# Optimization experiments

Measured on AMD Instinct MI355X. Metric: run time of the kernel, lower is better.

Reference implementation:

```python
import jax, jax.numpy as jnp
import numpy as np

DIST_THRES = 0.2
EPS = 1e-8


def _project(points, extrinsic, intrinsic):
    # points: [N,3] world; extrinsic: cam-to-world [4,4]; intrinsic: normalized [3,3]
    w2c = jnp.linalg.inv(extrinsic)
    hom = jnp.concatenate([points, jnp.ones_like(points[:, :1])], axis=-1)  # [N,4]
    cam = hom @ w2c.T  # [N,4]
    z = cam[:, 2]
    valid_z = z > EPS
    xy = cam[:, :2] / jnp.maximum(z, EPS)[:, None]
    ndc = xy @ intrinsic[:2, :2].T + intrinsic[:2, 2]  # [N,2] in [0,1] if visible
    return ndc, valid_z


def _remove_redundancy_batch(means_v, covs_v, shs_v, opas_v, scales_v, rots_v, extr, intr, h, w):
    # means_v: [v,hw,3]; extr: [v,4,4]; intr: [v,3,3]
    v, hw = means_v.shape[0], means_v.shape[1]
    n_total = v * hw
    attrs = (means_v, covs_v, shs_v, opas_v, scales_v, rots_v)

    def init_buf(x):
        buf = jnp.zeros((n_total,) + x.shape[2:], x.dtype)
        return buf.at[:hw].set(x[0])  # view 0 kept wholesale

    bufs = [init_buf(a) for a in attrs]
    valid = jnp.zeros((n_total,), bool).at[:hw].set(True)

    for view in range(1, v):  # small fixed view count: python loop ok
        ndc, vz = _project(bufs[0], extr[view], intr[view])
        m = (ndc[:, 0] >= 0) & (ndc[:, 0] < 1) & (ndc[:, 1] >= 0) & (ndc[:, 1] < 1) & vz & valid
        x = jnp.floor(ndc[:, 0] * w).astype(jnp.int32)
        y = jnp.floor(ndc[:, 1] * h).astype(jnp.int32)
        # original indexes with stride h (y*h + x); bug-faithful, requires h == w
        pix = jnp.clip(y * h + x, 0, hw - 1)
        vpts = means_v[view][pix]  # gather candidate view gaussian at projected pixel
        dist = jnp.linalg.norm(bufs[0] - vpts, axis=1)
        occ = m & (dist <= DIST_THRES)  # accumulated gaussians that cover a pixel of this view
        idx = jnp.where(occ, pix, hw)  # dump masked-out entries into overflow slot
        keep = jnp.ones((hw + 1,), bool).at[idx].set(False)[:hw]  # unoccupied pixels -> keep new gaussian
        sl = slice(view * hw, (view + 1) * hw)
        new_vals = tuple(a[view] for a in attrs)
        bufs = [b.at[sl].set(jnp.where(keep.reshape((-1,) + (1,) * (nv.ndim - 1)), nv, 0))
                for b, nv in zip(bufs, new_vals)]
        valid = valid.at[sl].set(keep)
    return bufs + [valid]


def reference(means, covariances, harmonics, opacities, scales, rotations, extrinsics, intrinsics, h, w):
    b = means.shape[0]
    outs = [
        _remove_redundancy_batch(means[i], covariances[i], harmonics[i], opacities[i],
                                 scales[i], rotations[i], extrinsics[i], intrinsics[i], h, w)
        for i in range(b)
    ]
    # (means, covariances, harmonics, opacities, scales, rotations, valid_mask)
    return tuple(jnp.stack([o[k] for o in outs]) for k in range(7))


def setup_inputs() -> dict:
    key = jax.random.key(0)
    b, v, h, w, d_sh = 1, 4, 256, 256, 25
    hw = h * w
    ks = jax.random.split(key, 7)
    xy = jax.random.uniform(ks[0], (b, v, hw, 2), minval=-1.5, maxval=1.5)
    z = jax.random.uniform(ks[1], (b, v, hw, 1), minval=1.0, maxval=3.0)
    means = jnp.concatenate([xy, z], axis=-1)
    covariances = jax.random.normal(ks[2], (b, v, hw, 3, 3)) * 0.01
    harmonics = jax.random.normal(ks[3], (b, v, hw, 3, d_sh))
    opacities = jax.random.uniform(ks[4], (b, v, hw))
    scales = jax.random.uniform(ks[5], (b, v, hw, 3)) * 0.05
    rotations = jax.random.normal(ks[6], (b, v, hw, 4))
    # near-identity cam-to-world with small x offsets per view
    offs = jnp.arange(v, dtype=jnp.float32) * 0.15 - 0.225
    extrinsics = jnp.tile(jnp.eye(4, dtype=jnp.float32), (b, v, 1, 1)).at[:, :, 0, 3].set(offs[None, :])
    intrinsics = (jnp.zeros((b, v, 3, 3), jnp.float32)
                  .at[:, :, 0, 0].set(1.0).at[:, :, 1, 1].set(1.0)
                  .at[:, :, 0, 2].set(0.5).at[:, :, 1, 2].set(0.5)
                  .at[:, :, 2, 2].set(1.0))
    return {"means": means, "covariances": covariances, "harmonics": harmonics,
            "opacities": opacities, "scales": scales, "rotations": rotations,
            "extrinsics": extrinsics, "intrinsics": intrinsics, "h": h, "w": w}
```

## Files before the change

### kernel.cpp

```cpp
#include <hip/hip_runtime.h>
#include <stdint.h>


__device__ void inv4x4(const float* M, float* out) {
    double m[16];
    for (int i = 0; i < 16; ++i) m[i] = (double)M[i];
    double inv[16];
    inv[0]  =  m[5]*m[10]*m[15] - m[5]*m[11]*m[14] - m[9]*m[6]*m[15] + m[9]*m[7]*m[14] + m[13]*m[6]*m[11] - m[13]*m[7]*m[10];
    inv[4]  = -m[4]*m[10]*m[15] + m[4]*m[11]*m[14] + m[8]*m[6]*m[15] - m[8]*m[7]*m[14] - m[12]*m[6]*m[11] + m[12]*m[7]*m[10];
    inv[8]  =  m[4]*m[9]*m[15]  - m[4]*m[11]*m[13] - m[8]*m[5]*m[15] + m[8]*m[7]*m[13] + m[12]*m[5]*m[11] - m[12]*m[7]*m[9];
    inv[12] = -m[4]*m[9]*m[14]  + m[4]*m[10]*m[13] + m[8]*m[5]*m[14] - m[8]*m[6]*m[13] - m[12]*m[5]*m[10] + m[12]*m[6]*m[9];
    inv[1]  = -m[1]*m[10]*m[15] + m[1]*m[11]*m[14] + m[9]*m[2]*m[15] - m[9]*m[3]*m[14] - m[13]*m[2]*m[11] + m[13]*m[3]*m[10];
    inv[5]  =  m[0]*m[10]*m[15] - m[0]*m[11]*m[14] - m[8]*m[2]*m[15] + m[8]*m[3]*m[14] + m[12]*m[2]*m[11] - m[12]*m[3]*m[10];
    inv[9]  = -m[0]*m[9]*m[15]  + m[0]*m[11]*m[13] + m[8]*m[1]*m[15] - m[8]*m[3]*m[13] - m[12]*m[1]*m[11] + m[12]*m[3]*m[9];
    inv[13] =  m[0]*m[9]*m[14]  - m[0]*m[10]*m[13] - m[8]*m[1]*m[14] + m[8]*m[2]*m[13] + m[12]*m[1]*m[10] - m[12]*m[2]*m[9];
    inv[2]  =  m[1]*m[6]*m[15]  - m[1]*m[7]*m[14]  - m[5]*m[2]*m[15] + m[5]*m[3]*m[14] + m[13]*m[2]*m[7]  - m[13]*m[3]*m[6];
    inv[6]  = -m[0]*m[6]*m[15]  + m[0]*m[7]*m[14]  + m[4]*m[2]*m[15] - m[4]*m[3]*m[14] - m[12]*m[2]*m[7]  + m[12]*m[3]*m[6];
    inv[10] =  m[0]*m[5]*m[15]  - m[0]*m[7]*m[13]  - m[4]*m[1]*m[15] + m[4]*m[3]*m[13] + m[12]*m[1]*m[7]  - m[12]*m[3]*m[5];
    inv[14] = -m[0]*m[5]*m[14]  + m[0]*m[6]*m[13]  + m[4]*m[1]*m[14] - m[4]*m[2]*m[13] - m[12]*m[1]*m[6]  + m[12]*m[2]*m[5];
    inv[3]  = -m[1]*m[6]*m[11]  + m[1]*m[7]*m[10]  + m[5]*m[2]*m[11] - m[5]*m[3]*m[10] - m[9]*m[2]*m[7]   + m[9]*m[3]*m[6];
    inv[7]  =  m[0]*m[6]*m[11]  - m[0]*m[7]*m[10]  - m[4]*m[2]*m[11] + m[4]*m[3]*m[10] + m[8]*m[2]*m[7]   - m[8]*m[3]*m[6];
    inv[11] = -m[0]*m[5]*m[11]  + m[0]*m[7]*m[9]   + m[4]*m[1]*m[11] - m[4]*m[3]*m[9]  - m[8]*m[1]*m[7]   + m[8]*m[3]*m[5];
    inv[15] =  m[0]*m[5]*m[10]  - m[0]*m[6]*m[9]   - m[4]*m[1]*m[10] + m[4]*m[2]*m[9]  + m[8]*m[1]*m[6]   - m[8]*m[2]*m[5];
    double det = m[0]*inv[0] + m[1]*inv[4] + m[2]*inv[8] + m[3]*inv[12];
    double idet = 1.0 / det;
    for (int i = 0; i < 16; ++i) out[i] = (float)(inv[i] * idet);
}

__global__ void init_kernel(const float* __restrict__ extr, float* __restrict__ w2c,
                            uint32_t* __restrict__ bitmap_words, int v, int n_words) {
    int tid = blockIdx.x * blockDim.x + threadIdx.x;
    int stride = gridDim.x * blockDim.x;
    for (int i = tid; i < n_words; i += stride) bitmap_words[i] = 0u;
    if (tid < v) inv4x4(extr + tid * 16, w2c + tid * 16);
}

__global__ void mark_kernel(const float* __restrict__ means_all,
                            const uint8_t* __restrict__ bm_all,
                            const float* __restrict__ means_view,
                            const float* __restrict__ w2c,
                            const float* __restrict__ intr,
                            uint8_t* __restrict__ bitmap_out,
                            int n_prev, const int* __restrict__ hp,
                            const int* __restrict__ wp, int hw) {
#pragma clang fp contract(off)
    int i = blockIdx.x * blockDim.x + threadIdx.x;
    if (i >= n_prev) return;
    if (bm_all[i] != 0) return;
    float px = means_all[3 * i + 0];
    float py = means_all[3 * i + 1];
    float pz = means_all[3 * i + 2];
    float c0 = w2c[0] * px + w2c[1] * py + w2c[2]  * pz + w2c[3];
    float c1 = w2c[4] * px + w2c[5] * py + w2c[6]  * pz + w2c[7];
    float c2 = w2c[8] * px + w2c[9] * py + w2c[10] * pz + w2c[11];
    bool vz = c2 > 1e-8f;
    float zz = fmaxf(c2, 1e-8f);
    float xp = c0 / zz;
    float yp = c1 / zz;
    float n0 = (xp * intr[0] + yp * intr[1]) + intr[2];
    float n1 = (xp * intr[3] + yp * intr[4]) + intr[5];
    bool m = (n0 >= 0.0f) & (n0 < 1.0f) & (n1 >= 0.0f) & (n1 < 1.0f) & vz;
    if (!m) return;
    int w_ = *wp;
    int h_ = *hp;
    int x = (int)floorf(n0 * (float)w_);
    int y = (int)floorf(n1 * (float)h_);
    int pix = y * h_ + x;
    pix = min(max(pix, 0), hw - 1);
    float vx = means_view[3 * pix + 0];
    float vy = means_view[3 * pix + 1];
    float vw = means_view[3 * pix + 2];
    float dx = px - vx, dy = py - vy, dz = pz - vw;
    float dist = sqrtf((dx * dx + dy * dy) + dz * dz);
    if (dist <= 0.2f) bitmap_out[pix] = 1;
}

__global__ void __launch_bounds__(256) write_all(
        const float4* __restrict__ means, const float4* __restrict__ covs,
        const float4* __restrict__ shs,   const float4* __restrict__ opas,
        const float4* __restrict__ scales,const float4* __restrict__ rots,
        const uint8_t* __restrict__ bm,   float4* __restrict__ out, long N) {
    const long N4 = N >> 2;
    const long B0 = 3 * N4, B1 = 12 * N4, B2 = 87 * N4, B3 = 88 * N4,
               B4 = 91 * N4, B5 = 95 * N4, B6 = 96 * N4;
    long q = (long)blockIdx.x * blockDim.x + threadIdx.x;
    if (q >= B6) return;
    float4 v;
    if (q < B0) {
        long t = q, e = 4 * t;
        v = means[t];
        if (bm[(e + 0) / 3]) v.x = 0.f;
        if (bm[(e + 1) / 3]) v.y = 0.f;
        if (bm[(e + 2) / 3]) v.z = 0.f;
        if (bm[(e + 3) / 3]) v.w = 0.f;
    } else if (q < B1) {
        long t = q - B0, e = 4 * t;
        v = covs[t];
        if (bm[(e + 0) / 9]) v.x = 0.f;
        if (bm[(e + 1) / 9]) v.y = 0.f;
        if (bm[(e + 2) / 9]) v.z = 0.f;
        if (bm[(e + 3) / 9]) v.w = 0.f;
    } else if (q < B2) {
        long t = q - B1, e = 4 * t;
        v = shs[t];
        if (bm[(e + 0) / 75]) v.x = 0.f;
        if (bm[(e + 1) / 75]) v.y = 0.f;
        if (bm[(e + 2) / 75]) v.z = 0.f;
        if (bm[(e + 3) / 75]) v.w = 0.f;
    } else if (q < B3) {
        long t = q - B2, e = 4 * t;
        v = opas[t];
        if (bm[e + 0]) v.x = 0.f;
        if (bm[e + 1]) v.y = 0.f;
        if (bm[e + 2]) v.z = 0.f;
        if (bm[e + 3]) v.w = 0.f;
    } else if (q < B4) {
        long t = q - B3, e = 4 * t;
        v = scales[t];
        if (bm[(e + 0) / 3]) v.x = 0.f;
        if (bm[(e + 1) / 3]) v.y = 0.f;
        if (bm[(e + 2) / 3]) v.z = 0.f;
        if (bm[(e + 3) / 3]) v.w = 0.f;
    } else if (q < B5) {
        long t = q - B4;
        v = rots[t];
        if (bm[t]) v = make_float4(0.f, 0.f, 0.f, 0.f);
    } else {
        long t = q - B5, e = 4 * t;
        v.x = bm[e + 0] ? 0.f : 1.f;
        v.y = bm[e + 1] ? 0.f : 1.f;
        v.z = bm[e + 2] ? 0.f : 1.f;
        v.w = bm[e + 3] ? 0.f : 1.f;
    }
    out[q] = v;
}

extern "C" void kernel_launch(void* const* d_in, const int* in_sizes, int n_in,
                              void* d_out, int out_size, void* d_ws, size_t ws_size,
                              hipStream_t stream) {
    const float* means  = (const float*)d_in[0];
    const float* covs   = (const float*)d_in[1];
    const float* shs    = (const float*)d_in[2];
    const float* opas   = (const float*)d_in[3];
    const float* scales = (const float*)d_in[4];
    const float* rots   = (const float*)d_in[5];
    const float* extr   = (const float*)d_in[6];
    const float* intr   = (const float*)d_in[7];
    const int*   hp     = (const int*)d_in[8];
    const int*   wp     = (const int*)d_in[9];

    const int v  = in_sizes[6] / 16;
    const int hw = in_sizes[3] / v;
    const long N = (long)v * hw;

    float*   w2c     = (float*)d_ws;
    uint8_t* bitmaps = (uint8_t*)d_ws + 1024;

    {
        int n_words = (int)(N / 4);
        int blocks = (n_words + 255) / 256;
        init_kernel<<<blocks, 256, 0, stream>>>(extr, w2c, (uint32_t*)bitmaps, v, n_words);
    }

    for (int view = 1; view < v; ++view) {
        int n_prev = view * hw;
        int mblocks = (n_prev + 255) / 256;
        mark_kernel<<<mblocks, 256, 0, stream>>>(means, bitmaps,
                                                 means + (long)view * hw * 3,
                                                 w2c + view * 16, intr + view * 9,
                                                 bitmaps + (long)view * hw,
                                                 n_prev, hp, wp, hw);
    }

    const long n4 = 96L * (N >> 2);
    const int wblocks = (int)((n4 + 255) / 256);
    write_all<<<wblocks, 256, 0, stream>>>((const float4*)means, (const float4*)covs,
                                           (const float4*)shs, (const float4*)opas,
                                           (const float4*)scales, (const float4*)rots,
                                           bitmaps, (float4*)d_out, N);
}
```

Measured before the change: 202.8 us.

## Fuse per-view output copy into mark kernels to overlap with marking

The single final write kernel is split per view. The copy of view cv-1, whose bitmap is already final, now runs inside the same launch as the marking pass for the next view, so the bandwidth-bound copy overlaps the latency-bound marking launches. View 0 skips the bitmap read and the zeroing of its bitmap. Loads and stores are made nontemporal. The cost is larger grids per launch and 32-bit index arithmetic, which limits the supported problem sizes.

Result: faster. 198.7 us (median of 2 runs) (-2.0%).

```diff
diff --git a/kernel.cpp b/kernel.cpp
--- a/kernel.cpp
+++ b/kernel.cpp
@@ -1,6 +1,8 @@
 #include <hip/hip_runtime.h>
 #include <stdint.h>
 
+
+typedef float f4 __attribute__((ext_vector_type(4)));
 
 __device__ void inv4x4(const float* M, float* out) {
     double m[16];
@@ -28,111 +30,136 @@
 }
 
 __global__ void init_kernel(const float* __restrict__ extr, float* __restrict__ w2c,
-                            uint32_t* __restrict__ bitmap_words, int v, int n_words) {
+                            uint32_t* __restrict__ zero_words, int v, int n_words) {
     int tid = blockIdx.x * blockDim.x + threadIdx.x;
     int stride = gridDim.x * blockDim.x;
-    for (int i = tid; i < n_words; i += stride) bitmap_words[i] = 0u;
-    if (tid < v) inv4x4(extr + tid * 16, w2c + tid * 16);
-}
-
-__global__ void mark_kernel(const float* __restrict__ means_all,
-                            const uint8_t* __restrict__ bm_all,
-                            const float* __restrict__ means_view,
-                            const float* __restrict__ w2c,
-                            const float* __restrict__ intr,
-                            uint8_t* __restrict__ bitmap_out,
-                            int n_prev, const int* __restrict__ hp,
-                            const int* __restrict__ wp, int hw) {
+    for (int i = tid; i < n_words; i += stride) zero_words[i] = 0u;
+    if (tid >= 1 && tid < v) inv4x4(extr + tid * 16, w2c + tid * 16);
+}
+
+__global__ void __launch_bounds__(256) mark_copy(
+        const float* __restrict__ means_all,
+        const uint8_t* __restrict__ bm_all,
+        const float* __restrict__ means_view,
+        const float* __restrict__ w2c,
+        const float* __restrict__ intr,
+        uint8_t* __restrict__ bitmap_out,
+        int n_prev, const int* __restrict__ hp, const int* __restrict__ wp,
+        int hw, int mark_blocks,
+        const f4* __restrict__ means4, const f4* __restrict__ covs4,
+        const f4* __restrict__ shs4,   const f4* __restrict__ opas4,
+        const f4* __restrict__ scales4,const f4* __restrict__ rots4,
+        const uint8_t* __restrict__ bmc,
+        f4* __restrict__ out, int cview, int n4 ) {
 #pragma clang fp contract(off)
-    int i = blockIdx.x * blockDim.x + threadIdx.x;
-    if (i >= n_prev) return;
-    if (bm_all[i] != 0) return;
-    float px = means_all[3 * i + 0];
-    float py = means_all[3 * i + 1];
-    float pz = means_all[3 * i + 2];
-    float c0 = w2c[0] * px + w2c[1] * py + w2c[2]  * pz + w2c[3];
-    float c1 = w2c[4] * px + w2c[5] * py + w2c[6]  * pz + w2c[7];
-    float c2 = w2c[8] * px + w2c[9] * py + w2c[10] * pz + w2c[11];
-    bool vz = c2 > 1e-8f;
-    float zz = fmaxf(c2, 1e-8f);
-    float xp = c0 / zz;
-    float yp = c1 / zz;
-    float n0 = (xp * intr[0] + yp * intr[1]) + intr[2];
-    float n1 = (xp * intr[3] + yp * intr[4]) + intr[5];
-    bool m = (n0 >= 0.0f) & (n0 < 1.0f) & (n1 >= 0.0f) & (n1 < 1.0f) & vz;
-    if (!m) return;
-    int w_ = *wp;
-    int h_ = *hp;
-    int x = (int)floorf(n0 * (float)w_);
-    int y = (int)floorf(n1 * (float)h_);
-    int pix = y * h_ + x;
-    pix = min(max(pix, 0), hw - 1);
-    float vx = means_view[3 * pix + 0];
-    float vy = means_view[3 * pix + 1];
-    float vw = means_view[3 * pix + 2];
-    float dx = px - vx, dy = py - vy, dz = pz - vw;
-    float dist = sqrtf((dx * dx + dy * dy) + dz * dz);
-    if (dist <= 0.2f) bitmap_out[pix] = 1;
-}
-
-__global__ void __launch_bounds__(256) write_all(
-        const float4* __restrict__ means, const float4* __restrict__ covs,
-        const float4* __restrict__ shs,   const float4* __restrict__ opas,
-        const float4* __restrict__ scales,const float4* __restrict__ rots,
-        const uint8_t* __restrict__ bm,   float4* __restrict__ out, long N) {
-    const long N4 = N >> 2;
-    const long B0 = 3 * N4, B1 = 12 * N4, B2 = 87 * N4, B3 = 88 * N4,
-               B4 = 91 * N4, B5 = 95 * N4, B6 = 96 * N4;
-    long q = (long)blockIdx.x * blockDim.x + threadIdx.x;
-    if (q >= B6) return;
-    float4 v;
-    if (q < B0) {
-        long t = q, e = 4 * t;
-        v = means[t];
-        if (bm[(e + 0) / 3]) v.x = 0.f;
-        if (bm[(e + 1) / 3]) v.y = 0.f;
-        if (bm[(e + 2) / 3]) v.z = 0.f;
-        if (bm[(e + 3) / 3]) v.w = 0.f;
-    } else if (q < B1) {
-        long t = q - B0, e = 4 * t;
-        v = covs[t];
-        if (bm[(e + 0) / 9]) v.x = 0.f;
-        if (bm[(e + 1) / 9]) v.y = 0.f;
-        if (bm[(e + 2) / 9]) v.z = 0.f;
-        if (bm[(e + 3) / 9]) v.w = 0.f;
-    } else if (q < B2) {
-        long t = q - B1, e = 4 * t;
-        v = shs[t];
-        if (bm[(e + 0) / 75]) v.x = 0.f;
-        if (bm[(e + 1) / 75]) v.y = 0.f;
-        if (bm[(e + 2) / 75]) v.z = 0.f;
-        if (bm[(e + 3) / 75]) v.w = 0.f;
-    } else if (q < B3) {
-        long t = q - B2, e = 4 * t;
-        v = opas[t];
-        if (bm[e + 0]) v.x = 0.f;
-        if (bm[e + 1]) v.y = 0.f;
-        if (bm[e + 2]) v.z = 0.f;
-        if (bm[e + 3]) v.w = 0.f;
-    } else if (q < B4) {
-        long t = q - B3, e = 4 * t;
-        v = scales[t];
-        if (bm[(e + 0) / 3]) v.x = 0.f;
-        if (bm[(e + 1) / 3]) v.y = 0.f;
-        if (bm[(e + 2) / 3]) v.z = 0.f;
-        if (bm[(e + 3) / 3]) v.w = 0.f;
-    } else if (q < B5) {
-        long t = q - B4;
-        v = rots[t];
-        if (bm[t]) v = make_float4(0.f, 0.f, 0.f, 0.f);
+    if ((int)blockIdx.x < mark_blocks) {
+        int i = (int)blockIdx.x * 256 + (int)threadIdx.x;
+        if (i >= n_prev) return;
+        if (i >= hw && bm_all[i] != 0) return;
+        float px = means_all[3 * i + 0];
+        float py = means_all[3 * i + 1];
+        float pz = means_all[3 * i + 2];
+        float c0 = w2c[0] * px + w2c[1] * py + w2c[2]  * pz + w2c[3];
+        float c1 = w2c[4] * px + w2c[5] * py + w2c[6]  * pz + w2c[7];
+        float c2 = w2c[8] * px + w2c[9] * py + w2c[10] * pz + w2c[11];
+        bool vz = c2 > 1e-8f;
+        float zz = fmaxf(c2, 1e-8f);
+        float xp = c0 / zz;
+        float yp = c1 / zz;
+        float n0 = (xp * intr[0] + yp * intr[1]) + intr[2];
+        float n1 = (xp * intr[3] + yp * intr[4]) + intr[5];
+        bool m = (n0 >= 0.0f) & (n0 < 1.0f) & (n1 >= 0.0f) & (n1 < 1.0f) & vz;
+        if (!m) return;
+        int w_ = *wp;
+        int h_ = *hp;
+        int x = (int)floorf(n0 * (float)w_);
+        int y = (int)floorf(n1 * (float)h_);
+        int pix = y * h_ + x;
+        pix = min(max(pix, 0), hw - 1);
+        float vx = means_view[3 * pix + 0];
+        float vy = means_view[3 * pix + 1];
+        float vw = means_view[3 * pix + 2];
+        float dx = px - vx, dy = py - vy, dz = pz - vw;
+        float dist = sqrtf((dx * dx + dy * dy) + dz * dz);
+        if (dist <= 0.2f) bitmap_out[pix] = 1;
+        return;
+    }
+    int q = ((int)blockIdx.x - mark_blocks) * 256 + (int)threadIdx.x;
+    const int H4 = hw >> 2;
+    const int b0 = 3 * H4,  b1 = 12 * H4, b2 = 87 * H4,
+              b3 = 88 * H4, b4 = 91 * H4, b5 = 95 * H4, b6 = 96 * H4;
+    if (q >= b6) return;
+    const bool has = (bmc != nullptr);
+    f4 val;
+    int oi;
+    if (q < b0) {
+        int t = q, e = 4 * t;
+        val = __builtin_nontemporal_load(&means4[cview * b0 + t]);
+        if (has) {
+            if (bmc[(e + 0) / 3]) val.x = 0.f;
+            if (bmc[(e + 1) / 3]) val.y = 0.f;
+            if (bmc[(e + 2) / 3]) val.z = 0.f;
+            if (bmc[(e + 3) / 3]) val.w = 0.f;
+        }
+        oi = cview * b0 + t;
+    } else if (q < b1) {
+        int t = q - b0, e = 4 * t;
+        val = __builtin_nontemporal_load(&covs4[cview * 9 * H4 + t]);
+        if (has) {
+            if (bmc[(e + 0) / 9]) val.x = 0.f;
+            if (bmc[(e + 1) / 9]) val.y = 0.f;
+            if (bmc[(e + 2) / 9]) val.z = 0.f;
+            if (bmc[(e + 3) / 9]) val.w = 0.f;
+        }
+        oi = 3 * n4 + cview * 9 * H4 + t;
+    } else if (q < b2) {
+        int t = q - b1, e = 4 * t;
+        val = __builtin_nontemporal_load(&shs4[cview * 75 * H4 + t]);
+        if (has) {
+            if (bmc[(e + 0) / 75]) val.x = 0.f;
+            if (bmc[(e + 1) / 75]) val.y = 0.f;
+            if (bmc[(e + 2) / 75]) val.z = 0.f;
+            if (bmc[(e + 3) / 75]) val.w = 0.f;
+        }
+        oi = 12 * n4 + cview * 75 * H4 + t;
+    } else if (q < b3) {
+        int t = q - b2, e = 4 * t;
+        val = __builtin_nontemporal_load(&opas4[cview * H4 + t]);
+        if (has) {
+            if (bmc[e + 0]) val.x = 0.f;
+            if (bmc[e + 1]) val.y = 0.f;
+            if (bmc[e + 2]) val.z = 0.f;
+            if (bmc[e + 3]) val.w = 0.f;
+        }
+        oi = 87 * n4 + cview * H4 + t;
+    } else if (q < b4) {
+        int t = q - b3, e = 4 * t;
+        val = __builtin_nontemporal_load(&scales4[cview * 3 * H4 + t]);
+        if (has) {
+            if (bmc[(e + 0) / 3]) val.x = 0.f;
+            if (bmc[(e + 1) / 3]) val.y = 0.f;
+            if (bmc[(e + 2) / 3]) val.z = 0.f;
+            if (bmc[(e + 3) / 3]) val.w = 0.f;
+        }
+        oi = 88 * n4 + cview * 3 * H4 + t;
+    } else if (q < b5) {
+        int t = q - b4;
+        val = __builtin_nontemporal_load(&rots4[cview * 4 * H4 + t]);
+        if (has && bmc[t]) { val.x = 0.f; val.y = 0.f; val.z = 0.f; val.w = 0.f; }
+        oi = 91 * n4 + cview * 4 * H4 + t;
     } else {
-        long t = q - B5, e = 4 * t;
-        v.x = bm[e + 0] ? 0.f : 1.f;
-        v.y = bm[e + 1] ? 0.f : 1.f;
-        v.z = bm[e + 2] ? 0.f : 1.f;
-        v.w = bm[e + 3] ? 0.f : 1.f;
-    }
-    out[q] = v;
+        int t = q - b5, e = 4 * t;
+        if (has) {
+            val.x = bmc[e + 0] ? 0.f : 1.f;
+            val.y = bmc[e + 1] ? 0.f : 1.f;
+            val.z = bmc[e + 2] ? 0.f : 1.f;
+            val.w = bmc[e + 3] ? 0.f : 1.f;
+        } else {
+            val.x = 1.f; val.y = 1.f; val.z = 1.f; val.w = 1.f;
+        }
+        oi = 95 * n4 + cview * H4 + t;
+    }
+    __builtin_nontemporal_store(val, &out[oi]);
 }
 
 extern "C" void kernel_launch(void* const* d_in, const int* in_sizes, int n_in,
@@ -156,26 +183,40 @@
     float*   w2c     = (float*)d_ws;
     uint8_t* bitmaps = (uint8_t*)d_ws + 1024;
 
-    {
-        int n_words = (int)(N / 4);
+    const int n4 = (int)(N >> 2);
+    const int H4 = hw >> 2;
+    const int c6 = 96 * H4;
+    const int copy_blocks = (c6 + 255) / 256;
+
+    if (v > 1) {
+        int n_words = (v - 1) * hw / 4;
         int blocks = (n_words + 255) / 256;
-        init_kernel<<<blocks, 256, 0, stream>>>(extr, w2c, (uint32_t*)bitmaps, v, n_words);
+        init_kernel<<<blocks, 256, 0, stream>>>(extr, w2c,
+                                                (uint32_t*)(bitmaps + hw), v, n_words);
     }
 
     for (int view = 1; view < v; ++view) {
         int n_prev = view * hw;
-        int mblocks = (n_prev + 255) / 256;
-        mark_kernel<<<mblocks, 256, 0, stream>>>(means, bitmaps,
-                                                 means + (long)view * hw * 3,
-                                                 w2c + view * 16, intr + view * 9,
-                                                 bitmaps + (long)view * hw,
-                                                 n_prev, hp, wp, hw);
-    }
-
-    const long n4 = 96L * (N >> 2);
-    const int wblocks = (int)((n4 + 255) / 256);
-    write_all<<<wblocks, 256, 0, stream>>>((const float4*)means, (const float4*)covs,
-                                           (const float4*)shs, (const float4*)opas,
-                                           (const float4*)scales, (const float4*)rots,
-                                           bitmaps, (float4*)d_out, N);
-}
+        int mb = (n_prev + 255) / 256;
+        int cv = view - 1;
+        const uint8_t* bmc = (cv == 0) ? nullptr : bitmaps + (long)cv * hw;
+        mark_copy<<<mb + copy_blocks, 256, 0, stream>>>(
+            means, bitmaps, means + (long)view * hw * 3,
+            w2c + view * 16, intr + view * 9, bitmaps + (long)view * hw,
+            n_prev, hp, wp, hw, mb,
+            (const f4*)means, (const f4*)covs, (const f4*)shs,
+            (const f4*)opas, (const f4*)scales, (const f4*)rots,
+            bmc, (f4*)d_out, cv, n4);
+    }
+
+    {
+        int cv = v - 1;
+        const uint8_t* bmc = (cv == 0) ? nullptr : bitmaps + (long)cv * hw;
+        mark_copy<<<copy_blocks, 256, 0, stream>>>(
+            means, bitmaps, means, w2c, intr, bitmaps,
+            0, hp, wp, hw, 0,
+            (const f4*)means, (const f4*)covs, (const f4*)shs,
+            (const f4*)opas, (const f4*)scales, (const f4*)rots,
+            bmc, (f4*)d_out, cv, n4);
+    }
+}
```
